# Performance work log

Measured on AMD Instinct MI355X. Metric: run time of the kernel, lower is better.

Reference implementation:

```python
import jax, jax.numpy as jnp
import numpy as np
import math

EPS = 1e-5
H = 8  # n_heads


def _layernorm(x, g, b):
    mu = jnp.mean(x, axis=-1, keepdims=True)
    var = jnp.var(x, axis=-1, keepdims=True)
    return (x - mu) * jax.lax.rsqrt(var + EPS) * g + b


def _conv1d(x_bdn, w_oik):
    # x: [B, D, N], w: [O, I, K] (torch Conv1d layout), padding = K//2
    k = w_oik.shape[-1]
    p = k // 2
    return jax.lax.conv_general_dilated(
        x_bdn, w_oik, window_strides=(1,), padding=((p, p),),
        dimension_numbers=('NCH', 'OIH', 'NCH'))


def setup_inputs() -> dict:
    key = jax.random.key(0)
    ks = jax.random.split(key, 10)
    B, N, D, dq = 4096, 25, 256, 64
    s = 0.02
    inp = {
        'x': jax.random.normal(ks[0], (B, N, D), jnp.float32),
        'wq': jax.random.normal(ks[1], (D, D, 3), jnp.float32) * s,
        'wk': jax.random.normal(ks[2], (D, D, 3), jnp.float32) * s,
        'wv': jax.random.normal(ks[3], (D, D, 3), jnp.float32) * s,
        'ln_q_g': jnp.ones((D,), jnp.float32), 'ln_q_b': jnp.zeros((D,), jnp.float32),
        'ln_k_g': jnp.ones((D,), jnp.float32), 'ln_k_b': jnp.zeros((D,), jnp.float32),
        'ln_v_g': jnp.ones((D,), jnp.float32), 'ln_v_b': jnp.zeros((D,), jnp.float32),
        'rel_table': jax.random.normal(ks[4], (2 * N - 1, H), jnp.float32) * s,
        'global_bias': jax.random.normal(ks[5], (H, N, N), jnp.float32) * s,
        'alpha': jnp.float32(1.0),
        'wqf': jax.random.normal(ks[6], (D, dq), jnp.float32) * s,
        'bqf': jnp.zeros((dq,), jnp.float32),
        'wqp': jax.random.normal(ks[7], (dq, H), jnp.float32) * s,
        'bqp': jnp.zeros((H,), jnp.float32),
        'wo': jax.random.normal(ks[8], (D, D), jnp.float32) * s,
        'bo': jnp.zeros((D,), jnp.float32),
    }
    return inp


def reference(x, wq, wk, wv, ln_q_g, ln_q_b, ln_k_g, ln_k_b, ln_v_g, ln_v_b,
              rel_table, global_bias, alpha, wqf, bqf, wqp, bqp, wo, bo):
    B, N, D = x.shape
    dk = D // H
    xp = jnp.transpose(x, (0, 2, 1))  # [B, D, N]

    # conv projections + LayerNorm + residual
    q = x + _layernorm(jnp.transpose(_conv1d(xp, wq), (0, 2, 1)), ln_q_g, ln_q_b)
    k = x + _layernorm(jnp.transpose(_conv1d(xp, wk), (0, 2, 1)), ln_k_g, ln_k_b)
    v = x + _layernorm(jnp.transpose(_conv1d(xp, wv), (0, 2, 1)), ln_v_g, ln_v_b)

    q4 = q.reshape(B, N, H, dk)
    k4 = k.reshape(B, N, H, dk)
    v4 = v.reshape(B, N, H, dk)

    scores = jnp.einsum('bnhd,bmhd->bhnm', q4, k4) / math.sqrt(dk)

    # relative position bias: table[(i - j) + N - 1] -> [H, N, N]
    ids = jnp.arange(N)
    rel_idx = ids[:, None] - ids[None, :] + N - 1  # [N, N]
    rel_bias = jnp.transpose(rel_table[rel_idx], (2, 0, 1))  # [H, N, N]
    scores = scores + rel_bias[None] + global_bias[None] * alpha

    # dynamic adjacency bias from pairwise node feature differences
    qf = x @ wqf + bqf  # [B, N, dq]
    pair = jnp.tanh(qf[:, :, None, :] - qf[:, None, :, :])  # [B, N, N, dq]
    dyn = pair @ wqp + bqp  # [B, N, N, H]
    scores = scores + jnp.transpose(dyn, (0, 3, 1, 2))

    attn = jax.nn.softmax(scores, axis=-1)  # [B, H, N, N]
    out = jnp.einsum('bhnm,bmhd->bnhd', attn, v4).reshape(B, N, D)
    return out @ wo + bo
```

## Files before the change

### kernel.cpp

```cpp
#include <hip/hip_runtime.h>
#include <hip/hip_bf16.h>
#include <stdint.h>

using u16 = unsigned short;
using u32 = unsigned int;

typedef __attribute__((ext_vector_type(8))) __bf16 bf16x8;
typedef __attribute__((ext_vector_type(4))) float f32x4;

__device__ __forceinline__ float bf2f(u16 h) {
  u32 u = ((u32)h) << 16;
  return __builtin_bit_cast(float, u);
}
__device__ __forceinline__ u16 f2bf(float f) {
  u32 u = __builtin_bit_cast(u32, f);
  u += 0x7fffu + ((u >> 16) & 1u);
  return (u16)(u >> 16);
}
__device__ __forceinline__ float blo(u32 u) { return __builtin_bit_cast(float, u << 16); }
__device__ __forceinline__ float bhi(u32 u) { return __builtin_bit_cast(float, u & 0xffff0000u); }

__device__ __forceinline__ uint4 cvt8(const float* s) {
  float4 f0 = *(const float4*)s;
  float4 f1 = *(const float4*)(s + 4);
  uint4 r;
  r.x = (u32)f2bf(f0.x) | ((u32)f2bf(f0.y) << 16);
  r.y = (u32)f2bf(f0.z) | ((u32)f2bf(f0.w) << 16);
  r.z = (u32)f2bf(f1.x) | ((u32)f2bf(f1.y) << 16);
  r.w = (u32)f2bf(f1.z) | ((u32)f2bf(f1.w) << 16);
  return r;
}

__device__ __forceinline__ u32 tanh2(u32 a, u32 b) {
  const float d0 = blo(a) - blo(b);
  const float d1 = bhi(a) - bhi(b);
  const float e0 = __expf(2.f * d0), e1 = __expf(2.f * d1);
  const float t0 = 1.f - 2.f * __builtin_amdgcn_rcpf(e0 + 1.f);
  const float t1 = 1.f - 2.f * __builtin_amdgcn_rcpf(e1 + 1.f);
  return (u32)f2bf(t0) | ((u32)f2bf(t1) << 16);
}

__device__ __forceinline__ void gl_lds(const u16* gsrc, u16* ldsbase) {
  __builtin_amdgcn_global_load_lds(
      (const __attribute__((address_space(1))) u32*)gsrc,
      (__attribute__((address_space(3))) u32*)ldsbase, 16, 0, 0);
}


__global__ __launch_bounds__(256) void prep_kernel(
    const float* __restrict__ wq, const float* __restrict__ wk, const float* __restrict__ wv,
    const float* __restrict__ wo, const float* __restrict__ wqf,
    const float* __restrict__ lnqg, const float* __restrict__ lnqb,
    const float* __restrict__ lnkg, const float* __restrict__ lnkb,
    const float* __restrict__ lnvg, const float* __restrict__ lnvb,
    const float* __restrict__ relt, const float* __restrict__ gbias,
    const float* __restrict__ alphap,
    const float* __restrict__ wqp, const float* __restrict__ bqp,
    const float* __restrict__ bqf, const float* __restrict__ bo,
    u16* __restrict__ wT, u16* __restrict__ woT,
    u16* __restrict__ wqfT, u16* __restrict__ params)
{
  long long j = (long long)blockIdx.x * 256 + threadIdx.x;
  if (j < 589824) {
    int col = (int)(j / 768), k = (int)(j % 768);
    int p = col >> 8, o = col & 255, t = k >> 8, i = k & 255;
    const float* w = (p == 0) ? wq : (p == 1) ? wk : wv;
    wT[j] = f2bf(w[o * 768 + i * 3 + t]);
    return;
  }
  j -= 589824;
  if (j < 65536) {
    int n = (int)(j >> 8), k = (int)(j & 255);
    woT[j] = f2bf(wo[k * 256 + n]);
    return;
  }
  j -= 65536;
  if (j < 16384) {
    int col = (int)(j >> 8), k = (int)(j & 255);
    wqfT[j] = f2bf(wqf[k * 64 + col]);
    return;
  }
  j -= 16384;
  if (j < 8864) {
    int t = (int)j;
    if (t >= 8800) { params[t] = 0; return; }
    if (t >= 7776) {
      int t2 = t - 7776;
      int col = t2 >> 6, k = t2 & 63;
      params[t] = (col < 8) ? f2bf(wqp[k * 8 + col]) : (u16)0;
      return;
    }
    if (t >= 1928 && t < 6928) {
      int idx = t - 1928;
      int h = idx / 625, rem = idx % 625, n = rem / 25, m = rem % 25;
      params[t] = f2bf(gbias[idx] * alphap[0] + relt[(n - m + 24) * 8 + h] + bqp[h]);
      return;
    }
    const float* src; int si;
    if (t < 1536) {
      int a = t >> 8, c = t & 255;
      src = (a == 0) ? lnqg : (a == 1) ? lnqb : (a == 2) ? lnkg
          : (a == 3) ? lnkb : (a == 4) ? lnvg : lnvb;
      si = c;
    } else if (t < 1928) { src = relt;  si = t - 1536; }
    else if (t < 6936)   { src = alphap; si = 0; }
    else if (t < 7448)   { src = wqp;   si = t - 6936; }
    else if (t < 7456)   { src = bqp;   si = t - 7448; }
    else if (t < 7520)   { src = bqf;   si = t - 7456; }
    else                 { src = bo;    si = t - 7520; }
    params[t] = f2bf(src[si]);
  }
}

__global__ __launch_bounds__(256) void xconv_kernel(
    const float* __restrict__ x, u16* __restrict__ xbf)
{
  const long long i = ((long long)blockIdx.x * 256 + threadIdx.x) * 8;
  *(uint4*)&xbf[i] = cvt8(x + i);
}

__global__ __launch_bounds__(512) void convln_kernel(
    const u16* __restrict__ xbf, long long row0,
    const u16* __restrict__ wT, const u16* __restrict__ wqfT,
    u16* __restrict__ C,
    u16* __restrict__ qfc,
    const u16* __restrict__ params,
    const u16* __restrict__ zpad)
{
  __shared__ __align__(16) u16 Asm[128 * 64];
  __shared__ __align__(16) u16 Bsm[256 * 64];
  __shared__ float sG[256];
  __shared__ float sB[256];
  __shared__ float sSum[4][128];
  __shared__ float sSq[4][128];

  const int tid = threadIdx.x;
  const int l = tid & 63, w = tid >> 6;
  const int p = blockIdx.x;
  const int r0 = blockIdx.y * 128;
  const int lrow = l >> 3, chunk = l & 7;
  const int g8 = (l >> 4) * 8, l15 = l & 15;
  const int rbase = 4 * (l >> 4);
  const int swz = l15 & 7;

  if (p < 3) {
    const int c0 = p * 256;
    if (tid < 256) sG[tid] = bf2f(params[p * 512 + tid]);
    else           sB[tid - 256] = bf2f(params[p * 512 + 256 + (tid - 256)]);
    const int wr = w >> 2, wc = w & 3;

    f32x4 acc[4][4];
#pragma unroll
    for (int m = 0; m < 4; ++m)
#pragma unroll
      for (int n = 0; n < 4; ++n)
        acc[m][n] = (f32x4){0.f, 0.f, 0.f, 0.f};

    for (int ks = 0; ks < 12; ++ks) {
      const int k0 = ks * 64;
      const int t = k0 >> 8, kc = k0 & 255;
      __syncthreads();
#pragma unroll
      for (int it = 0; it < 2; ++it) {
        const int seg = w * 2 + it;
        const int row_l = seg * 8 + lrow;
        const bool valid = ((unsigned)((r0 + row_l) % 25 + t - 1) < 25u);
        const u16* src = valid
            ? xbf + (size_t)(row0 + r0 + row_l + t - 1) * 256 + kc + ((chunk ^ lrow) << 3)
            : zpad;
        gl_lds(src, &Asm[seg * 512]);
      }
#pragma unroll
      for (int it = 0; it < 4; ++it) {
        const int seg = w * 4 + it;
        const int row_l = seg * 8 + lrow;
        const u16* src = wT + (size_t)(c0 + row_l) * 768 + k0 + ((chunk ^ lrow) << 3);
        gl_lds(src, &Bsm[seg * 512]);
      }
      __syncthreads();

#pragma unroll
      for (int kk = 0; kk < 64; kk += 32) {
        const int c = (kk >> 3) + (l >> 4);
        const int co = ((c ^ swz) << 3);
        bf16x8 av[4], bv[4];
#pragma unroll
        for (int m = 0; m < 4; ++m)
          av[m] = *(const bf16x8*)&Asm[(wr * 64 + m * 16 + l15) * 64 + co];
#pragma unroll
        for (int n = 0; n < 4; ++n)
          bv[n] = *(const bf16x8*)&Bsm[(wc * 64 + n * 16 + l15) * 64 + co];
#pragma unroll
        for (int m = 0; m < 4; ++m)
#pragma unroll
          for (int n = 0; n < 4; ++n)
            acc[m][n] = __builtin_amdgcn_mfma_f32_16x16x32_bf16(av[m], bv[n], acc[m][n], 0, 0, 0);
      }
    }

#pragma unroll
    for (int m = 0; m < 4; ++m) {
#pragma unroll
      for (int r = 0; r < 4; ++r) {
        float s = 0.f, q = 0.f;
#pragma unroll
        for (int n = 0; n < 4; ++n) { const float v = acc[m][n][r]; s += v; q += v * v; }
#pragma unroll
        for (int mk = 1; mk < 16; mk <<= 1) {
          s += __shfl_xor(s, mk, 64);
          q += __shfl_xor(q, mk, 64);
        }
        if (l15 == 0) {
          const int row = wr * 64 + m * 16 + rbase + r;
          sSum[wc][row] = s;
          sSq[wc][row] = q;
        }
      }
    }
    __syncthreads();

#pragma unroll
    for (int m = 0; m < 4; ++m) {
      float mu4[4], rs4[4];
#pragma unroll
      for (int r = 0; r < 4; ++r) {
        const int row = wr * 64 + m * 16 + rbase + r;
        const float tot = sSum[0][row] + sSum[1][row] + sSum[2][row] + sSum[3][row];
        const float tq  = sSq[0][row] + sSq[1][row] + sSq[2][row] + sSq[3][row];
        const float mu = tot * (1.f / 256.f);
        const float var = tq * (1.f / 256.f) - mu * mu;
        mu4[r] = mu;
        rs4[r] = rsqrtf(var + 1e-5f);
      }
#pragma unroll
      for (int n = 0; n < 4; ++n) {
        const int lc = wc * 64 + n * 16 + l15;
        const float g = sG[lc], bb = sB[lc];
#pragma unroll
        for (int r = 0; r < 4; ++r) {
          const int row = wr * 64 + m * 16 + rbase + r;
          const float xv = bf2f(xbf[(size_t)(row0 + r0 + row) * 256 + lc]);
          const float v = (acc[m][n][r] - mu4[r]) * rs4[r] * g + bb + xv;
          C[(size_t)(r0 + row) * 768 + c0 + lc] = f2bf(v);
        }
      }
    }
  } else {
    f32x4 acc2[4];
#pragma unroll
    for (int n = 0; n < 4; ++n) acc2[n] = (f32x4){0.f, 0.f, 0.f, 0.f};

    for (int ks2 = 0; ks2 < 4; ++ks2) {
      __syncthreads();
#pragma unroll
      for (int it = 0; it < 2; ++it) {
        const int seg = w * 2 + it;
        const int row_l = seg * 8 + lrow;
        const u16* src = xbf + (size_t)(row0 + r0 + row_l) * 256 + ks2 * 64
                       + ((chunk ^ lrow) << 3);
        gl_lds(src, &Asm[seg * 512]);
      }
      {
        const int row_l = w * 8 + lrow;
        const u16* src = wqfT + (size_t)row_l * 256 + ks2 * 64 + ((chunk ^ lrow) << 3);
        gl_lds(src, &Bsm[w * 512]);
      }
      __syncthreads();

#pragma unroll
      for (int kk = 0; kk < 64; kk += 32) {
        const int c = (kk >> 3) + (l >> 4);
        const int co = ((c ^ swz) << 3);
        const bf16x8 av = *(const bf16x8*)&Asm[(w * 16 + l15) * 64 + co];
#pragma unroll
        for (int n = 0; n < 4; ++n) {
          const bf16x8 bv = *(const bf16x8*)&Bsm[(n * 16 + l15) * 64 + co];
          acc2[n] = __builtin_amdgcn_mfma_f32_16x16x32_bf16(av, bv, acc2[n], 0, 0, 0);
        }
      }
    }
#pragma unroll
    for (int n = 0; n < 4; ++n) {
      const int col = n * 16 + l15;
      const float badd = bf2f(params[7456 + col]);
#pragma unroll
      for (int r = 0; r < 4; ++r) {
        const int row = r0 + w * 16 + rbase + r;
        qfc[(size_t)row * 64 + col] = f2bf(acc2[n][r] + badd);
      }
    }
  }
}

template<int BN, bool HAS_BIAS, bool F32OUT>
__global__ __launch_bounds__(256) void gemm_kernel(
    const u16* __restrict__ A, int lda, long long row0,
    const u16* __restrict__ BT, int ldb,
    void* __restrict__ Cv, int ldc,
    const u16* __restrict__ bias,
    int ksteps)
{
  constexpr int NB = BN / 32;
  __shared__ __align__(16) u16 Asm[128 * 64];
  __shared__ __align__(16) u16 Bsm[BN * 64];

  const int tid = threadIdx.x;
  const int l = tid & 63;
  const int w = tid >> 6;
  const int c0 = blockIdx.x * BN;
  const int r0 = blockIdx.y * 128;
  const int wr = w >> 1, wc = w & 1;

  f32x4 acc[4][NB];
#pragma unroll
  for (int m = 0; m < 4; ++m)
#pragma unroll
    for (int n = 0; n < NB; ++n)
      acc[m][n] = (f32x4){0.f, 0.f, 0.f, 0.f};

  const int lrow = l >> 3;
  const int chunk = l & 7;
  const int l15 = l & 15;
  const int swz = l15 & 7;

  for (int ks = 0; ks < ksteps; ++ks) {
    const int k0 = ks * 64;
    __syncthreads();
#pragma unroll
    for (int it = 0; it < 4; ++it) {
      const int seg = w * 4 + it;
      const int row_l = seg * 8 + lrow;
      const u16* src = A + (size_t)(row0 + r0 + row_l) * lda + k0 + ((chunk ^ lrow) << 3);
      gl_lds(src, &Asm[seg * 512]);
    }
#pragma unroll
    for (int it = 0; it < NB; ++it) {
      const int seg = w * NB + it;
      const int row_l = seg * 8 + lrow;
      const u16* src = BT + (size_t)(c0 + row_l) * ldb + k0 + ((chunk ^ lrow) << 3);
      gl_lds(src, &Bsm[seg * 512]);
    }
    __syncthreads();

#pragma unroll
    for (int kk = 0; kk < 64; kk += 32) {
      const int c = (kk >> 3) + (l >> 4);
      const int co = ((c ^ swz) << 3);
      bf16x8 av[4], bv[NB];
#pragma unroll
      for (int m = 0; m < 4; ++m)
        av[m] = *(const bf16x8*)&Asm[(wr * 64 + m * 16 + l15) * 64 + co];
#pragma unroll
      for (int n = 0; n < NB; ++n)
        bv[n] = *(const bf16x8*)&Bsm[(wc * (BN / 2) + n * 16 + l15) * 64 + co];
#pragma unroll
      for (int m = 0; m < 4; ++m)
#pragma unroll
        for (int n = 0; n < NB; ++n)
          acc[m][n] = __builtin_amdgcn_mfma_f32_16x16x32_bf16(av[m], bv[n], acc[m][n], 0, 0, 0);
    }
  }

  const int rbase = 4 * (l >> 4);
#pragma unroll
  for (int m = 0; m < 4; ++m) {
#pragma unroll
    for (int n = 0; n < NB; ++n) {
      const int col = c0 + wc * (BN / 2) + n * 16 + l15;
      float badd = 0.f;
      if (HAS_BIAS) badd = bf2f(bias[col]);
#pragma unroll
      for (int r = 0; r < 4; ++r) {
        const int row = r0 + wr * 64 + m * 16 + rbase + r;
        const float v = acc[m][n][r] + badd;
        if constexpr (F32OUT) ((float*)Cv)[(size_t)row * ldc + col] = v;
        else                  ((u16*)Cv)[(size_t)row * ldc + col] = f2bf(v);
      }
    }
  }
}

__global__ __launch_bounds__(256) void attn_kernel(
    u16* __restrict__ qkv,
    const u16* __restrict__ qf,
    const u16* __restrict__ params)
{
  __shared__ __align__(16) char arena[38848];
  float* sS    = (float*)arena;
  u16*   sV    = (u16*)(arena + 20000);
  u16*   sQF   = (u16*)(arena + 33200);
  u16*   sWQPT = (u16*)(arena + 36800);

  const int b = blockIdx.x;
  const int tid = threadIdx.x;
  const int w = tid >> 6, l = tid & 63;
  const int g8 = (l >> 4) * 8;
  const int rbase = 4 * (l >> 4);
  const int l15 = l & 15;

  {
    for (int i = tid; i < 800; i += 256) {
      const int m = i >> 5, c8 = (i & 31) * 8;
      *(uint4*)&sV[m * 264 + c8] =
          *(const uint4*)(qkv + (size_t)(b * 25 + m) * 768 + 512 + c8);
    }
    for (int i = tid; i < 200; i += 256) {
      const int r = i >> 3, c8 = (i & 7) * 8;
      *(uint4*)&sQF[r * 72 + c8] = *(const uint4*)(qf + (size_t)b * 1600 + r * 64 + c8);
    }
    for (int i = tid; i < 128; i += 256)
      ((uint4*)sWQPT)[i] = ((const uint4*)(params + 7776))[i];
  }
  __syncthreads();

  f32x4 dt[10];
  {
    const bf16x8 bv0 = *(const bf16x8*)&sWQPT[l15 * 64 + g8];
    const bf16x8 bv1 = *(const bf16x8*)&sWQPT[l15 * 64 + 32 + g8];
#pragma unroll
    for (int ti = 0; ti < 10; ++ti) {
      const int p0 = (ti * 4 + w) * 16;
      int p = p0 + l15; if (p > 624) p = 624;
      const int n = p / 25, m = p % 25;
      const uint4 qn0 = *(const uint4*)&sQF[n * 72 + g8];
      const uint4 qn1 = *(const uint4*)&sQF[n * 72 + 32 + g8];
      const uint4 qm0 = *(const uint4*)&sQF[m * 72 + g8];
      const uint4 qm1 = *(const uint4*)&sQF[m * 72 + 32 + g8];
      u32 a0[4], a1[4];
      a0[0] = tanh2(qn0.x, qm0.x); a0[1] = tanh2(qn0.y, qm0.y);
      a0[2] = tanh2(qn0.z, qm0.z); a0[3] = tanh2(qn0.w, qm0.w);
      a1[0] = tanh2(qn1.x, qm1.x); a1[1] = tanh2(qn1.y, qm1.y);
      a1[2] = tanh2(qn1.z, qm1.z); a1[3] = tanh2(qn1.w, qm1.w);
      const bf16x8 av0 = __builtin_bit_cast(bf16x8, *(uint4*)a0);
      const bf16x8 av1 = __builtin_bit_cast(bf16x8, *(uint4*)a1);
      f32x4 d = (f32x4){0.f, 0.f, 0.f, 0.f};
      d = __builtin_amdgcn_mfma_f32_16x16x32_bf16(av0, bv0, d, 0, 0, 0);
      d = __builtin_amdgcn_mfma_f32_16x16x32_bf16(av1, bv1, d, 0, 0, 0);
      dt[ti] = d;
    }
    bf16x8 zf8;
#pragma unroll
    for (int j = 0; j < 8; ++j) zf8[j] = (__bf16)0.f;
#pragma unroll
    for (int hh = 0; hh < 2; ++hh) {
      const int h = 2 * w + hh;
      bf16x8 qa[2], kb[2];
#pragma unroll
      for (int t = 0; t < 2; ++t) {
        const int row = l15 + 16 * t;
        if (row < 25) {
          const u16* base = qkv + (size_t)(b * 25 + row) * 768 + h * 32 + g8;
          qa[t] = *(const bf16x8*)base;
          kb[t] = *(const bf16x8*)(base + 256);
        } else { qa[t] = zf8; kb[t] = zf8; }
      }
#pragma unroll
      for (int tn = 0; tn < 2; ++tn)
#pragma unroll
        for (int tm = 0; tm < 2; ++tm) {
          f32x4 d = __builtin_amdgcn_mfma_f32_16x16x32_bf16(
              qa[tn], kb[tm], (f32x4){0.f, 0.f, 0.f, 0.f}, 0, 0, 0);
          const int m = l15 + 16 * tm;
#pragma unroll
          for (int r = 0; r < 4; ++r) {
            const int n = rbase + r + 16 * tn;
            if (n < 25 && m < 25) {
              const int idx = h * 625 + n * 25 + m;
              sS[idx] = d[r] * 0.17677669529663687f + bf2f(params[1928 + idx]);
            }
          }
        }
    }
  }
  __syncthreads();

  {
    if (l15 < 8) {
      const int h = l15;
#pragma unroll
      for (int ti = 0; ti < 10; ++ti) {
        const int p0 = (ti * 4 + w) * 16;
#pragma unroll
        for (int r = 0; r < 4; ++r) {
          const int p = p0 + rbase + r;
          if (p < 625) sS[h * 625 + p] += dt[ti][r];
        }
      }
    }
  }
  __syncthreads();

  {
    for (int u = tid; u < 200; u += 256) {
      const int h = u / 25, n = u % 25;
      float* rp = &sS[h * 625 + n * 25];
      float mx = -1e30f;
#pragma unroll
      for (int m = 0; m < 25; ++m) mx = fmaxf(mx, rp[m]);
      float ssum = 0.f;
#pragma unroll
      for (int m = 0; m < 25; ++m) { rp[m] = __expf(rp[m] - mx); ssum += rp[m]; }
      const float inv = __builtin_amdgcn_rcpf(ssum);
#pragma unroll
      for (int m = 0; m < 25; ++m) rp[m] *= inv;
    }
  }
  __syncthreads();

  {
#pragma unroll
    for (int hh = 0; hh < 2; ++hh) {
      const int h = 2 * w + hh;
      bf16x8 pa[2], vb[2];
#pragma unroll
      for (int t = 0; t < 2; ++t) {
        const int n = l15 + 16 * t;
#pragma unroll
        for (int j = 0; j < 8; ++j) {
          const int m = g8 + j;
          const float pv = (n < 25 && m < 25) ? sS[h * 625 + n * 25 + m] : 0.f;
          pa[t][j] = (__bf16)pv;
        }
      }
#pragma unroll
      for (int t = 0; t < 2; ++t) {
        const int dcol = l15 + 16 * t;
#pragma unroll
        for (int j = 0; j < 8; ++j) {
          const int m = g8 + j;
          vb[t][j] = (m < 25)
              ? __builtin_bit_cast(__bf16, sV[m * 264 + h * 32 + dcol])
              : (__bf16)0.f;
        }
      }
#pragma unroll
      for (int tn = 0; tn < 2; ++tn)
#pragma unroll
        for (int td = 0; td < 2; ++td) {
          f32x4 d = __builtin_amdgcn_mfma_f32_16x16x32_bf16(
              pa[tn], vb[td], (f32x4){0.f, 0.f, 0.f, 0.f}, 0, 0, 0);
          const int dcol = l15 + 16 * td;
#pragma unroll
          for (int r = 0; r < 4; ++r) {
            const int n = rbase + r + 16 * tn;
            if (n < 25)
              qkv[(size_t)(b * 25 + n) * 768 + h * 32 + dcol] = f2bf(d[r]);
          }
        }
    }
  }
}

extern "C" void kernel_launch(void* const* d_in, const int* in_sizes, int n_in,
                              void* d_out, int out_size, void* d_ws, size_t ws_size,
                              hipStream_t stream) {
  (void)in_sizes; (void)n_in; (void)out_size;
  const float* x    = (const float*)d_in[0];
  const float* wq   = (const float*)d_in[1];
  const float* wk   = (const float*)d_in[2];
  const float* wv   = (const float*)d_in[3];
  const float* lnqg = (const float*)d_in[4];
  const float* lnqb = (const float*)d_in[5];
  const float* lnkg = (const float*)d_in[6];
  const float* lnkb = (const float*)d_in[7];
  const float* lnvg = (const float*)d_in[8];
  const float* lnvb = (const float*)d_in[9];
  const float* relt = (const float*)d_in[10];
  const float* gbias= (const float*)d_in[11];
  const float* alph = (const float*)d_in[12];
  const float* wqf  = (const float*)d_in[13];
  const float* bqf  = (const float*)d_in[14];
  const float* wqp  = (const float*)d_in[15];
  const float* bqp  = (const float*)d_in[16];
  const float* wo   = (const float*)d_in[17];
  const float* bo   = (const float*)d_in[18];

  char* ws = (char*)d_ws;
  u16* params = (u16*)(ws + 0);
  u16* wT     = (u16*)(ws + 32768);
  u16* woT    = (u16*)(ws + 1212416);
  u16* wqfT   = (u16*)(ws + 1343488);
  const size_t fixed_bytes = 1376256;
  const size_t xbf_bytes = 52428800;
  const size_t per_batch = 41600;
  u16* zpad = params + 8800;

  int CB = 4096;
  while (CB > 128 && fixed_bytes + xbf_bytes + (size_t)CB * per_batch > ws_size) CB >>= 1;
  const int nchunks = 4096 / CB;
  const int rows = CB * 25;

  u16* x_bf = (u16*)(ws + fixed_bytes);
  const size_t chunk_off = fixed_bytes + xbf_bytes;
  u16* qkv_c = (u16*)(ws + chunk_off);
  u16* qf_c  = (u16*)(ws + chunk_off + (size_t)CB * 38400);
  float* outf = (float*)d_out;

  prep_kernel<<<2659, 256, 0, stream>>>(
      wq, wk, wv, wo, wqf, lnqg, lnqb, lnkg, lnkb, lnvg, lnvb,
      relt, gbias, alph, wqp, bqp, bqf, bo,
      wT, woT, wqfT, params);
  xconv_kernel<<<12800, 256, 0, stream>>>(x, x_bf);

  for (int c = 0; c < nchunks; ++c) {
    const long long R0 = (long long)c * rows;

    convln_kernel<<<dim3(4, rows / 128), 512, 0, stream>>>(
        x_bf, R0, wT, wqfT, qkv_c, qf_c, params, zpad);

    attn_kernel<<<CB, 256, 0, stream>>>(qkv_c, qf_c, params);

    gemm_kernel<128, true, true><<<dim3(2, rows / 128), 256, 0, stream>>>(
        qkv_c, 768, 0, woT, 256, outf + (size_t)R0 * 256, 256, params + 7520, 4);
  }
}
```

Measured before the change: 415.4 us.

## Reuse one haloed activation tile across the three conv taps

The conv+LayerNorm kernel used to treat the 3-tap convolution as a K=768 GEMM, reloading a shifted activation tile for each tap and using a zero-pad buffer for boundaries. It now loads one 136-row tile (128 rows plus halo) per K slice, along with all three tap weight slabs. The taps become row-offset reads from LDS, and sequence boundaries are handled by register masks. This cuts activation global loads and barrier rounds by a factor of three, but raises LDS use to over 110 KB per block, which likely limits each CU to one block.

```diff
diff --git a/kernel.cpp b/kernel.cpp
--- a/kernel.cpp
+++ b/kernel.cpp
@@ -124,11 +124,10 @@
     const u16* __restrict__ wT, const u16* __restrict__ wqfT,
     u16* __restrict__ C,
     u16* __restrict__ qfc,
-    const u16* __restrict__ params,
-    const u16* __restrict__ zpad)
+    const u16* __restrict__ params)
 {
-  __shared__ __align__(16) u16 Asm[128 * 64];
-  __shared__ __align__(16) u16 Bsm[256 * 64];
+  __shared__ __align__(16) u16 Asm[136 * 64];
+  __shared__ __align__(16) u16 Bsm[3 * 256 * 64];
   __shared__ float sG[256];
   __shared__ float sB[256];
   __shared__ float sSum[4][128];
@@ -139,15 +138,27 @@
   const int p = blockIdx.x;
   const int r0 = blockIdx.y * 128;
   const int lrow = l >> 3, chunk = l & 7;
-  const int g8 = (l >> 4) * 8, l15 = l & 15;
+  const int l15 = l & 15;
   const int rbase = 4 * (l >> 4);
-  const int swz = l15 & 7;
+  const int cbase = l >> 4;
+
+  bf16x8 zf8;
+#pragma unroll
+  for (int j = 0; j < 8; ++j) zf8[j] = (__bf16)0.f;
 
   if (p < 3) {
     const int c0 = p * 256;
+    const int wr = w >> 2, wc = w & 3;
     if (tid < 256) sG[tid] = bf2f(params[p * 512 + tid]);
     else           sB[tid - 256] = bf2f(params[p * 512 + 256 + (tid - 256)]);
-    const int wr = w >> 2, wc = w & 3;
+
+    bool m0[4], m2[4];
+#pragma unroll
+    for (int m = 0; m < 4; ++m) {
+      const int n25 = (r0 + wr * 64 + m * 16 + l15) % 25;
+      m0[m] = (n25 != 0);
+      m2[m] = (n25 != 24);
+    }
 
     f32x4 acc[4][4];
 #pragma unroll
@@ -156,45 +167,44 @@
       for (int n = 0; n < 4; ++n)
         acc[m][n] = (f32x4){0.f, 0.f, 0.f, 0.f};
 
-    for (int ks = 0; ks < 12; ++ks) {
-      const int k0 = ks * 64;
-      const int t = k0 >> 8, kc = k0 & 255;
+    for (int ki = 0; ki < 4; ++ki) {
       __syncthreads();
-#pragma unroll
-      for (int it = 0; it < 2; ++it) {
-        const int seg = w * 2 + it;
-        const int row_l = seg * 8 + lrow;
-        const bool valid = ((unsigned)((r0 + row_l) % 25 + t - 1) < 25u);
-        const u16* src = valid
-            ? xbf + (size_t)(row0 + r0 + row_l + t - 1) * 256 + kc + ((chunk ^ lrow) << 3)
-            : zpad;
-        gl_lds(src, &Asm[seg * 512]);
-      }
-#pragma unroll
-      for (int it = 0; it < 4; ++it) {
-        const int seg = w * 4 + it;
-        const int row_l = seg * 8 + lrow;
-        const u16* src = wT + (size_t)(c0 + row_l) * 768 + k0 + ((chunk ^ lrow) << 3);
-        gl_lds(src, &Bsm[seg * 512]);
+      for (int s = w; s < 17; s += 8) {
+        const long long R = (long long)row0 + r0 - 1 + s * 8 + lrow;
+        const u16* src = xbf + R * 256 + ki * 64 + ((chunk ^ lrow) << 3);
+        gl_lds(src, &Asm[s * 512]);
+      }
+      for (int s = w; s < 96; s += 8) {
+        const int t = s >> 5, st = s & 31;
+        const u16* src = wT + (size_t)(c0 + st * 8 + lrow) * 768 + t * 256 + ki * 64
+                       + ((chunk ^ lrow) << 3);
+        gl_lds(src, &Bsm[s * 512]);
       }
       __syncthreads();
 
 #pragma unroll
-      for (int kk = 0; kk < 64; kk += 32) {
-        const int c = (kk >> 3) + (l >> 4);
-        const int co = ((c ^ swz) << 3);
-        bf16x8 av[4], bv[4];
-#pragma unroll
-        for (int m = 0; m < 4; ++m)
-          av[m] = *(const bf16x8*)&Asm[(wr * 64 + m * 16 + l15) * 64 + co];
-#pragma unroll
-        for (int n = 0; n < 4; ++n)
-          bv[n] = *(const bf16x8*)&Bsm[(wc * 64 + n * 16 + l15) * 64 + co];
-#pragma unroll
-        for (int m = 0; m < 4; ++m)
+      for (int kk = 0; kk < 2; ++kk) {
+        const int c = kk * 4 + cbase;
+#pragma unroll
+        for (int t = 0; t < 3; ++t) {
+          const int sa = (l15 + t) & 7;
+          const int sb = l15 & 7;
+          bf16x8 av[4], bv[4];
+#pragma unroll
+          for (int m = 0; m < 4; ++m) {
+            av[m] = *(const bf16x8*)&Asm[(wr * 64 + m * 16 + l15 + t) * 64 + ((c ^ sa) << 3)];
+            if (t == 0) av[m] = m0[m] ? av[m] : zf8;
+            if (t == 2) av[m] = m2[m] ? av[m] : zf8;
+          }
 #pragma unroll
           for (int n = 0; n < 4; ++n)
-            acc[m][n] = __builtin_amdgcn_mfma_f32_16x16x32_bf16(av[m], bv[n], acc[m][n], 0, 0, 0);
+            bv[n] = *(const bf16x8*)&Bsm[(t * 256 + wc * 64 + n * 16 + l15) * 64 + ((c ^ sb) << 3)];
+#pragma unroll
+          for (int m = 0; m < 4; ++m)
+#pragma unroll
+            for (int n = 0; n < 4; ++n)
+              acc[m][n] = __builtin_amdgcn_mfma_f32_16x16x32_bf16(av[m], bv[n], acc[m][n], 0, 0, 0);
+        }
       }
     }
 
@@ -250,31 +260,28 @@
 #pragma unroll
     for (int n = 0; n < 4; ++n) acc2[n] = (f32x4){0.f, 0.f, 0.f, 0.f};
 
-    for (int ks2 = 0; ks2 < 4; ++ks2) {
+    for (int ki = 0; ki < 4; ++ki) {
       __syncthreads();
-#pragma unroll
-      for (int it = 0; it < 2; ++it) {
-        const int seg = w * 2 + it;
-        const int row_l = seg * 8 + lrow;
-        const u16* src = xbf + (size_t)(row0 + r0 + row_l) * 256 + ks2 * 64
-                       + ((chunk ^ lrow) << 3);
-        gl_lds(src, &Asm[seg * 512]);
+      for (int s = w; s < 17; s += 8) {
+        const long long R = (long long)row0 + r0 - 1 + s * 8 + lrow;
+        const u16* src = xbf + R * 256 + ki * 64 + ((chunk ^ lrow) << 3);
+        gl_lds(src, &Asm[s * 512]);
       }
       {
-        const int row_l = w * 8 + lrow;
-        const u16* src = wqfT + (size_t)row_l * 256 + ks2 * 64 + ((chunk ^ lrow) << 3);
-        gl_lds(src, &Bsm[w * 512]);
+        const int s = w;
+        const u16* src = wqfT + (size_t)(s * 8 + lrow) * 256 + ki * 64 + ((chunk ^ lrow) << 3);
+        gl_lds(src, &Bsm[s * 512]);
       }
       __syncthreads();
 
 #pragma unroll
-      for (int kk = 0; kk < 64; kk += 32) {
-        const int c = (kk >> 3) + (l >> 4);
-        const int co = ((c ^ swz) << 3);
-        const bf16x8 av = *(const bf16x8*)&Asm[(w * 16 + l15) * 64 + co];
+      for (int kk = 0; kk < 2; ++kk) {
+        const int c = kk * 4 + cbase;
+        const int sa = (l15 + 1) & 7, sb = l15 & 7;
+        const bf16x8 av = *(const bf16x8*)&Asm[(w * 16 + l15 + 1) * 64 + ((c ^ sa) << 3)];
 #pragma unroll
         for (int n = 0; n < 4; ++n) {
-          const bf16x8 bv = *(const bf16x8*)&Bsm[(n * 16 + l15) * 64 + co];
+          const bf16x8 bv = *(const bf16x8*)&Bsm[(n * 16 + l15) * 64 + ((c ^ sb) << 3)];
           acc2[n] = __builtin_amdgcn_mfma_f32_16x16x32_bf16(av, bv, acc2[n], 0, 0, 0);
         }
       }
@@ -583,7 +590,6 @@
   const size_t fixed_bytes = 1376256;
   const size_t xbf_bytes = 52428800;
   const size_t per_batch = 41600;
-  u16* zpad = params + 8800;
 
   int CB = 4096;
   while (CB > 128 && fixed_bytes + xbf_bytes + (size_t)CB * per_batch > ws_size) CB >>= 1;
@@ -606,7 +612,7 @@
     const long long R0 = (long long)c * rows;
 
     convln_kernel<<<dim3(4, rows / 128), 512, 0, stream>>>(
-        x_bf, R0, wT, wqfT, qkv_c, qf_c, params, zpad);
+        x_bf, R0, wT, wqfT, qkv_c, qf_c, params);
 
     attn_kernel<<<CB, 256, 0, stream>>>(qkv_c, qf_c, params);
 
```

New measurement: 451.1 us. +8.6%, slower.

## Make each convln block handle 64 rows across all projections

Applied to the files above, without the earlier changes.

Reorganizes the conv+LayerNorm kernel. Before, separate 512-thread blocks each handled one projection (q, k, v or qf) for 128 rows. Now each 256-thread block takes 64 rows and loops over the three conv projections, then computes the qf GEMM. LayerNorm gamma/beta for all three projections are staged in shared memory once per block. The change aims for better locality of the input rows and smaller per-block LDS, at the cost of fewer blocks in flight and more serial work inside each block.

```diff
diff --git a/kernel.cpp b/kernel.cpp
--- a/kernel.cpp
+++ b/kernel.cpp
@@ -119,7 +119,7 @@
   *(uint4*)&xbf[i] = cvt8(x + i);
 }
 
-__global__ __launch_bounds__(512) void convln_kernel(
+__global__ __launch_bounds__(256) void convln_kernel(
     const u16* __restrict__ xbf, long long row0,
     const u16* __restrict__ wT, const u16* __restrict__ wqfT,
     u16* __restrict__ C,
@@ -127,27 +127,29 @@
     const u16* __restrict__ params,
     const u16* __restrict__ zpad)
 {
-  __shared__ __align__(16) u16 Asm[128 * 64];
+  __shared__ __align__(16) u16 Asm[64 * 64];
   __shared__ __align__(16) u16 Bsm[256 * 64];
-  __shared__ float sG[256];
-  __shared__ float sB[256];
-  __shared__ float sSum[4][128];
-  __shared__ float sSq[4][128];
+  __shared__ float sG3[768];
+  __shared__ float sB3[768];
+  __shared__ float sSum[4][64];
+  __shared__ float sSq[4][64];
 
   const int tid = threadIdx.x;
   const int l = tid & 63, w = tid >> 6;
-  const int p = blockIdx.x;
-  const int r0 = blockIdx.y * 128;
+  const int r0 = blockIdx.x * 64;
   const int lrow = l >> 3, chunk = l & 7;
-  const int g8 = (l >> 4) * 8, l15 = l & 15;
+  const int l15 = l & 15;
   const int rbase = 4 * (l >> 4);
   const int swz = l15 & 7;
 
-  if (p < 3) {
+  for (int i = tid; i < 768; i += 256) {
+    const int pp = i >> 8, cc = i & 255;
+    sG3[i] = bf2f(params[pp * 512 + cc]);
+    sB3[i] = bf2f(params[pp * 512 + 256 + cc]);
+  }
+
+  for (int p = 0; p < 3; ++p) {
     const int c0 = p * 256;
-    if (tid < 256) sG[tid] = bf2f(params[p * 512 + tid]);
-    else           sB[tid - 256] = bf2f(params[p * 512 + 256 + (tid - 256)]);
-    const int wr = w >> 2, wc = w & 3;
 
     f32x4 acc[4][4];
 #pragma unroll
@@ -171,8 +173,8 @@
         gl_lds(src, &Asm[seg * 512]);
       }
 #pragma unroll
-      for (int it = 0; it < 4; ++it) {
-        const int seg = w * 4 + it;
+      for (int it = 0; it < 8; ++it) {
+        const int seg = w * 8 + it;
         const int row_l = seg * 8 + lrow;
         const u16* src = wT + (size_t)(c0 + row_l) * 768 + k0 + ((chunk ^ lrow) << 3);
         gl_lds(src, &Bsm[seg * 512]);
@@ -186,10 +188,10 @@
         bf16x8 av[4], bv[4];
 #pragma unroll
         for (int m = 0; m < 4; ++m)
-          av[m] = *(const bf16x8*)&Asm[(wr * 64 + m * 16 + l15) * 64 + co];
+          av[m] = *(const bf16x8*)&Asm[(m * 16 + l15) * 64 + co];
 #pragma unroll
         for (int n = 0; n < 4; ++n)
-          bv[n] = *(const bf16x8*)&Bsm[(wc * 64 + n * 16 + l15) * 64 + co];
+          bv[n] = *(const bf16x8*)&Bsm[(w * 64 + n * 16 + l15) * 64 + co];
 #pragma unroll
         for (int m = 0; m < 4; ++m)
 #pragma unroll
@@ -211,9 +213,9 @@
           q += __shfl_xor(q, mk, 64);
         }
         if (l15 == 0) {
-          const int row = wr * 64 + m * 16 + rbase + r;
-          sSum[wc][row] = s;
-          sSq[wc][row] = q;
+          const int row = m * 16 + rbase + r;
+          sSum[w][row] = s;
+          sSq[w][row] = q;
         }
       }
     }
@@ -224,7 +226,7 @@
       float mu4[4], rs4[4];
 #pragma unroll
       for (int r = 0; r < 4; ++r) {
-        const int row = wr * 64 + m * 16 + rbase + r;
+        const int row = m * 16 + rbase + r;
         const float tot = sSum[0][row] + sSum[1][row] + sSum[2][row] + sSum[3][row];
         const float tq  = sSq[0][row] + sSq[1][row] + sSq[2][row] + sSq[3][row];
         const float mu = tot * (1.f / 256.f);
@@ -234,36 +236,41 @@
       }
 #pragma unroll
       for (int n = 0; n < 4; ++n) {
-        const int lc = wc * 64 + n * 16 + l15;
-        const float g = sG[lc], bb = sB[lc];
+        const int lc = w * 64 + n * 16 + l15;
+        const float g = sG3[p * 256 + lc], bb = sB3[p * 256 + lc];
 #pragma unroll
         for (int r = 0; r < 4; ++r) {
-          const int row = wr * 64 + m * 16 + rbase + r;
+          const int row = m * 16 + rbase + r;
           const float xv = bf2f(xbf[(size_t)(row0 + r0 + row) * 256 + lc]);
           const float v = (acc[m][n][r] - mu4[r]) * rs4[r] * g + bb + xv;
           C[(size_t)(r0 + row) * 768 + c0 + lc] = f2bf(v);
         }
       }
     }
-  } else {
+    __syncthreads();
+  }
+
+  {
     f32x4 acc2[4];
 #pragma unroll
     for (int n = 0; n < 4; ++n) acc2[n] = (f32x4){0.f, 0.f, 0.f, 0.f};
 
-    for (int ks2 = 0; ks2 < 4; ++ks2) {
+    for (int ki = 0; ki < 4; ++ki) {
       __syncthreads();
 #pragma unroll
       for (int it = 0; it < 2; ++it) {
         const int seg = w * 2 + it;
         const int row_l = seg * 8 + lrow;
-        const u16* src = xbf + (size_t)(row0 + r0 + row_l) * 256 + ks2 * 64
+        const u16* src = xbf + (size_t)(row0 + r0 + row_l) * 256 + ki * 64
                        + ((chunk ^ lrow) << 3);
         gl_lds(src, &Asm[seg * 512]);
       }
-      {
-        const int row_l = w * 8 + lrow;
-        const u16* src = wqfT + (size_t)row_l * 256 + ks2 * 64 + ((chunk ^ lrow) << 3);
-        gl_lds(src, &Bsm[w * 512]);
+#pragma unroll
+      for (int it = 0; it < 2; ++it) {
+        const int seg = w * 2 + it;
+        const int row_l = seg * 8 + lrow;
+        const u16* src = wqfT + (size_t)row_l * 256 + ki * 64 + ((chunk ^ lrow) << 3);
+        gl_lds(src, &Bsm[seg * 512]);
       }
       __syncthreads();
 
@@ -605,7 +612,7 @@
   for (int c = 0; c < nchunks; ++c) {
     const long long R0 = (long long)c * rows;
 
-    convln_kernel<<<dim3(4, rows / 128), 512, 0, stream>>>(
+    convln_kernel<<<rows / 64, 256, 0, stream>>>(
         x_bf, R0, wT, wqfT, qkv_c, qf_c, params, zpad);
 
     attn_kernel<<<CB, 256, 0, stream>>>(qkv_c, qf_c, params);
```

New measurement: 716.5 us. 72.5% more time.
